# Optimization experiments

Measured on AMD Instinct MI355X. Metric: run time of the kernel, lower is better.

The kernel has to match this reference:

```python
import jax, jax.numpy as jnp
import numpy as np

S = 3072        # total packed tokens
E = 1280        # d_model
H = 20          # encoder_attention_heads
D = E // H      # head_dim = 64
NSEG = 16       # number of packed audio chunks


def setup_inputs() -> dict:
    key = jax.random.key(0)
    ks = jax.random.split(key, 9)
    w = lambda k, shape: (jax.random.normal(k, shape, jnp.float32) * 0.02)
    hidden_states = jax.random.normal(ks[0], (S, E), jnp.float32)
    cu_seqlens = (jnp.arange(NSEG + 1, dtype=jnp.int32) * (S // NSEG))
    return {
        "hidden_states": hidden_states,
        "Wq": w(ks[1], (E, E)), "bq": w(ks[2], (E,)),
        "Wk": w(ks[3], (E, E)),                      # k_proj has no bias
        "Wv": w(ks[4], (E, E)), "bv": w(ks[5], (E,)),
        "Wo": w(ks[6], (E, E)), "bo": w(ks[7], (E,)),
        "cu_seqlens": cu_seqlens,
    }


def reference(hidden_states, Wq, bq, Wk, Wv, bv, Wo, bo, cu_seqlens):
    Sq, Em = hidden_states.shape
    Dh = Em // H
    # projections (torch Linear: x @ W.T + b)
    q = (hidden_states @ Wq.T + bq).reshape(Sq, H, Dh).transpose(1, 0, 2)  # [H,S,D]
    k = (hidden_states @ Wk.T).reshape(Sq, H, Dh).transpose(1, 0, 2)       # [H,S,D]
    v = (hidden_states @ Wv.T + bv).reshape(Sq, H, Dh).transpose(1, 0, 2)  # [H,S,D]
    # block-diagonal additive mask from cu_seqlens (vectorized equivalent of
    # the original Python loop): tokens attend only within their own segment.
    pos = jnp.arange(Sq)
    seg = jnp.searchsorted(cu_seqlens[1:], pos, side="right")              # segment id per token
    same = seg[:, None] == seg[None, :]                                    # [S,S]
    bias = jnp.where(same, 0.0, jnp.finfo(q.dtype).min)
    attn = jnp.einsum("hqd,hkd->hqk", q, k) / np.sqrt(Dh).astype(q.dtype)  # [H,S,S]
    attn = jax.nn.softmax(attn + bias, axis=-1)
    out = jnp.einsum("hqk,hkd->hqd", attn, v)                              # [H,S,D]
    out = out.transpose(1, 0, 2).reshape(Sq, Em)
    return out @ Wo.T + bo
```

## Files before the change

kernel.cpp:

```cpp
#include <hip/hip_runtime.h>
#include <hip/hip_bf16.h>
#include <stdint.h>

#define S_TOK 3072
#define E_DIM 1280
#define H_NUM 20
#define D_HEAD 64
#define NSEG 16

typedef __attribute__((ext_vector_type(8))) short short8;
typedef __attribute__((ext_vector_type(4))) float f32x4;

__device__ __forceinline__ unsigned short f2bf(float f){
  union { float f; unsigned int i; } u; u.f = f;
  unsigned int r = u.i + 0x7FFFu + ((u.i >> 16) & 1u);
  return (unsigned short)(r >> 16);
}

__device__ __forceinline__ void gload_lds16(const void* g, void* l){
  __builtin_amdgcn_global_load_lds((__attribute__((address_space(1))) void*)(g),
                                   (__attribute__((address_space(3))) void*)(l), 16, 0, 0);
}

__global__ void cvt_all(const float* __restrict__ hs,
                        const float* __restrict__ w0, const float* __restrict__ w1,
                        const float* __restrict__ w2,
                        unsigned short* __restrict__ hsb,
                        unsigned short* __restrict__ dqkv,
                        int nHS4, int nW4){
  int i = blockIdx.x * blockDim.x + threadIdx.x;
  const float* src;
  unsigned short* dst;
  size_t sj, dj;
  if (i < nHS4){
    src = hs; dst = hsb; sj = i; dj = i;
  } else {
    int t = i - nHS4;
    int w = t / nW4;
    if (w >= 3) return;
    int j = t - w * nW4;
    src = (w == 0) ? w0 : (w == 1) ? w1 : w2;
    sj = j;
    dst = dqkv; dj = (size_t)w * nW4 + j;
  }
  float4 v = reinterpret_cast<const float4*>(src)[sj];
  ushort4 o;
  o.x = f2bf(v.x); o.y = f2bf(v.y); o.z = f2bf(v.z); o.w = f2bf(v.w);
  reinterpret_cast<ushort4*>(dst)[dj] = o;
}

template<int MODE, int BLOCK>
__global__ __launch_bounds__(BLOCK, 2) void gemm_k64(
    const unsigned short* __restrict__ A,
    const unsigned short* __restrict__ Bp,
    const float* __restrict__ bias0,
    const float* __restrict__ bias1,
    unsigned short* __restrict__ Oq,
    unsigned short* __restrict__ Ok,
    unsigned short* __restrict__ Ov,
    float* __restrict__ Of,
    int M, int N, int K)
{
  constexpr int BM = (MODE == 0) ? 256 : 128;
  constexpr int BN = BM;
  constexpr int WN = (MODE == 0) ? 4 : 2;
  constexpr int WM = (BLOCK / 64) / WN;
  constexpr int MR = BM / WM / 16;
  constexpr int NR = BN / WN / 16;
  constexpr int SLOT = (BM + BN) * 64;

  __shared__ __align__(16) unsigned short SH[2 * SLOT];

  const int nbn = N >> (MODE == 0 ? 8 : 7);
  const int sgn = nbn / 5;
  const int st = blockIdx.x / 20, ii = blockIdx.x % 20;
  const int bm = (st / sgn) * 4 + ii / 5;
  const int bn = (st % sgn) * 5 + ii % 5;
  const int row0 = bm * BM;
  const int col0 = bn * BN;

  const int tid  = threadIdx.x;
  const int lane = tid & 63;
  const int w    = tid >> 6;
  const int wm   = (MODE == 0) ? (w >> 2) : (w >> 1);
  const int wn   = (MODE == 0) ? (w & 3) : (w & 1);

  const f32x4 fz = {0.f, 0.f, 0.f, 0.f};
  f32x4 acc[MR][NR];
#pragma unroll
  for (int m = 0; m < MR; ++m)
#pragma unroll
    for (int n = 0; n < NR; ++n) acc[m][n] = fz;

  auto stage = [&](int buf, int t){
    unsigned short* base = SH + buf * SLOT;
    const int k0 = t << 6;
#pragma unroll
    for (int i = 0; i < 8; ++i){
      int s = i * BLOCK + tid;
      int r = s >> 3, p = s & 7;
      int ks = p ^ (r & 7);
      const unsigned short* g = (r < BM)
          ? A  + (size_t)(row0 + r) * K + k0 + ks * 8
          : Bp + (size_t)(col0 + (r - BM)) * K + k0 + ks * 8;
      gload_lds16(g, base + s * 8);
    }
  };

  const int nk = K >> 6;
  stage(0, 0);
  int buf = 0;
  for (int t = 0; t < nk; ++t){
    asm volatile("s_waitcnt vmcnt(0)" ::: "memory");
    __builtin_amdgcn_s_barrier();
    if (t + 1 < nk) stage(buf ^ 1, t + 1);

    const unsigned short* As = SH + buf * SLOT;
    const unsigned short* Bs = As + BM * 64;
    short8 af[MR][2], bf[NR][2];
#pragma unroll
    for (int n = 0; n < NR; ++n){
      int rb = wn * (BN / WN) + n * 16 + (lane & 15);
#pragma unroll
      for (int kk = 0; kk < 2; ++kk){
        int slot = kk * 4 + (lane >> 4);
        bf[n][kk] = *reinterpret_cast<const short8*>(&Bs[rb * 64 + ((slot ^ (rb & 7))) * 8]);
      }
    }
#pragma unroll
    for (int m = 0; m < MR; ++m){
      int ra = wm * (BM / WM) + m * 16 + (lane & 15);
#pragma unroll
      for (int kk = 0; kk < 2; ++kk){
        int slot = kk * 4 + (lane >> 4);
        af[m][kk] = *reinterpret_cast<const short8*>(&As[ra * 64 + ((slot ^ (ra & 7))) * 8]);
      }
    }
    __builtin_amdgcn_s_setprio(1);
#pragma unroll
    for (int kk = 0; kk < 2; ++kk)
#pragma unroll
      for (int m = 0; m < MR; ++m)
#pragma unroll
        for (int n = 0; n < NR; ++n)
          acc[m][n] = __builtin_amdgcn_mfma_f32_16x16x32_bf16(af[m][kk], bf[n][kk], acc[m][n], 0, 0, 0);
    __builtin_amdgcn_s_setprio(0);
    buf ^= 1;
  }
  __syncthreads();

  if (MODE == 0){
    unsigned short* Cs = SH;
    const int CSTR = 264;
    const int mat = col0 / E_DIM;
    const int cc0 = col0 - mat * E_DIM;
    unsigned short* dst = (mat == 0) ? Oq : ((mat == 1) ? Ok : Ov);
    float bb[NR];
#pragma unroll
    for (int n = 0; n < NR; ++n){
      int cc = cc0 + wn * 64 + n * 16 + (lane & 15);
      bb[n] = (mat == 0) ? bias0[cc] : (mat == 2 ? bias1[cc] : 0.0f);
    }
#pragma unroll
    for (int ph = 0; ph < 2; ++ph){
      if (wm == ph){
#pragma unroll
        for (int m = 0; m < MR; ++m)
#pragma unroll
          for (int n = 0; n < NR; ++n)
#pragma unroll
            for (int j = 0; j < 4; ++j){
              int rr = m * 16 + (lane >> 4) * 4 + j;
              int c  = wn * 64 + n * 16 + (lane & 15);
              Cs[rr * CSTR + c] = f2bf(acc[m][n][j] + bb[n]);
            }
      }
      __syncthreads();
#pragma unroll
      for (int i = 0; i < 8; ++i){
        int tk  = i * 512 + tid;
        int p   = tk >> 10;
        int idx = tk & 1023;
        int rr  = idx >> 3, sq = idx & 7;
        short8 vv = *reinterpret_cast<const short8*>(&Cs[rr * CSTR + p * 64 + sq * 8]);
        int gr = row0 + ph * 128 + rr;
        int hh = (cc0 >> 6) + p;
        *reinterpret_cast<short8*>(&dst[((size_t)hh * S_TOK + gr) * D_HEAD + sq * 8]) = vv;
      }
      __syncthreads();
    }
  } else {
#pragma unroll
    for (int m = 0; m < MR; ++m)
#pragma unroll
      for (int n = 0; n < NR; ++n){
        int c = col0 + wn * 64 + n * 16 + (lane & 15);
        float b = bias0[c];
#pragma unroll
        for (int j = 0; j < 4; ++j){
          int r = row0 + wm * 64 + m * 16 + (lane >> 4) * 4 + j;
          Of[(size_t)r * E_DIM + c] = acc[m][n][j] + b;
        }
      }
  }
}

#define VSTR 200
#define PSTR 72
#define ATTN_BLKS (H_NUM * NSEG * 3)
__global__ __launch_bounds__(256, 3) void attn_kernel(
    const unsigned short* __restrict__ Q,
    const unsigned short* __restrict__ Kb,
    const unsigned short* __restrict__ V,
    const int* __restrict__ cu,
    unsigned short* __restrict__ O,
    const float* __restrict__ Wo,
    unsigned short* __restrict__ wob,
    int nW4)
{
  __shared__ __align__(16) unsigned short Vt[64*VSTR];
  __shared__ __align__(16) unsigned short Pw[4][16][PSTR];

  const int bid  = blockIdx.x;
  if (bid >= ATTN_BLKS){
    int i = (bid - ATTN_BLKS) * 256 + threadIdx.x;
    if (i < nW4){
      float4 v = reinterpret_cast<const float4*>(Wo)[i];
      ushort4 o;
      o.x = f2bf(v.x); o.y = f2bf(v.y); o.z = f2bf(v.z); o.w = f2bf(v.w);
      reinterpret_cast<ushort4*>(wob)[i] = o;
    }
    return;
  }
  const int unit = bid / 3;
  const int third= bid - unit*3;
  const int h    = unit >> 4;
  const int seg  = unit & 15;
  const int s0   = cu[seg];
  const int L    = cu[seg + 1] - s0;
  if (L <= 0) return;

  const int tid  = threadIdx.x;
  const int lane = tid & 63;
  const int w    = tid >> 6;
  const int row0g = third*64 + w*16;

  const unsigned short* qh = Q  + (size_t)h * S_TOK * D_HEAD;
  const unsigned short* kh = Kb + (size_t)h * S_TOK * D_HEAD;
  const unsigned short* vh = V  + (size_t)h * S_TOK * D_HEAD;

#pragma unroll
  for (int i = 0; i < 6; ++i){
    int task = i*256 + tid;
    int sr   = task % 192;
    int grp  = task / 192;
    int svr  = s0 + (sr < L ? sr : L - 1);
    short8 vv = *reinterpret_cast<const short8*>(vh + (size_t)svr*64 + grp*8);
#pragma unroll
    for (int j = 0; j < 8; ++j) Vt[(grp*8 + j)*VSTR + sr] = (unsigned short)vv[j];
  }

  short8 qf[2];
#pragma unroll
  for (int kk = 0; kk < 2; ++kk){
    int r  = row0g + (lane & 15);
    int sr = s0 + (r < L ? r : L - 1);
    qf[kk] = *reinterpret_cast<const short8*>(qh + (size_t)sr*64 + kk*32 + (lane >> 4)*8);
  }

  __syncthreads();

  const f32x4 fz = {0.f, 0.f, 0.f, 0.f};
  const float SCL = 0.125f * 1.44269504088896f;

  f32x4 sacc[12];
#pragma unroll
  for (int nt = 0; nt < 12; ++nt) sacc[nt] = fz;

#pragma unroll
  for (int nt = 0; nt < 12; ++nt){
    int rb = nt*16 + (lane & 15);
    int sr = s0 + (rb < L ? rb : L - 1);
    const unsigned short* kr = kh + (size_t)sr*64 + (lane >> 4)*8;
    short8 kf0 = *reinterpret_cast<const short8*>(kr);
    short8 kf1 = *reinterpret_cast<const short8*>(kr + 32);
    sacc[nt] = __builtin_amdgcn_mfma_f32_16x16x32_bf16(qf[0], kf0, sacc[nt], 0, 0, 0);
    sacc[nt] = __builtin_amdgcn_mfma_f32_16x16x32_bf16(qf[1], kf1, sacc[nt], 0, 0, 0);
  }

  float rinv[4];
#pragma unroll
  for (int j = 0; j < 4; ++j){
    float mx = -1e30f;
#pragma unroll
    for (int nt = 0; nt < 12; ++nt){
      int c = nt*16 + (lane & 15);
      float vv = (c < L) ? sacc[nt][j] : -1e30f;
      sacc[nt][j] = vv;
      mx = fmaxf(mx, vv);
    }
    mx = fmaxf(mx, __shfl_xor(mx, 1, 64));
    mx = fmaxf(mx, __shfl_xor(mx, 2, 64));
    mx = fmaxf(mx, __shfl_xor(mx, 4, 64));
    mx = fmaxf(mx, __shfl_xor(mx, 8, 64));
    float sum = 0.f;
#pragma unroll
    for (int nt = 0; nt < 12; ++nt){
      float pp = exp2f((sacc[nt][j] - mx) * SCL);
      sacc[nt][j] = pp;
      sum += pp;
    }
    sum += __shfl_xor(sum, 1, 64);
    sum += __shfl_xor(sum, 2, 64);
    sum += __shfl_xor(sum, 4, 64);
    sum += __shfl_xor(sum, 8, 64);
    rinv[j] = 1.0f / sum;
  }

  f32x4 oacc[4];
#pragma unroll
  for (int nt = 0; nt < 4; ++nt) oacc[nt] = fz;

#pragma unroll
  for (int kk = 0; kk < 6; ++kk){
#pragma unroll
    for (int ntl = 0; ntl < 2; ++ntl){
      int nt = kk*2 + ntl;
#pragma unroll
      for (int j = 0; j < 4; ++j)
        Pw[w][(lane >> 4)*4 + j][ntl*16 + (lane & 15)] = f2bf(sacc[nt][j]);
    }
    short8 pf = *reinterpret_cast<const short8*>(&Pw[w][lane & 15][(lane >> 4)*8]);
#pragma unroll
    for (int nt4 = 0; nt4 < 4; ++nt4){
      int dcol = nt4*16 + (lane & 15);
      short8 vf = *reinterpret_cast<const short8*>(&Vt[dcol*VSTR + kk*32 + (lane >> 4)*8]);
      oacc[nt4] = __builtin_amdgcn_mfma_f32_16x16x32_bf16(pf, vf, oacc[nt4], 0, 0, 0);
    }
  }

#pragma unroll
  for (int nt4 = 0; nt4 < 4; ++nt4)
#pragma unroll
    for (int j = 0; j < 4; ++j)
      Pw[w][(lane >> 4)*4 + j][nt4*16 + (lane & 15)] = f2bf(oacc[nt4][j] * rinv[j]);

  {
    int r = lane >> 2;
    int gr = row0g + r;
    if (gr < L){
#pragma unroll
      for (int part = 0; part < 2; ++part){
        int c0 = (lane & 3)*16 + part*8;
        short8 vv = *reinterpret_cast<const short8*>(&Pw[w][r][c0]);
        *reinterpret_cast<short8*>(&O[(size_t)(s0 + gr) * E_DIM + h*64 + c0]) = vv;
      }
    }
  }
}

extern "C" void kernel_launch(void* const* d_in, const int* in_sizes, int n_in,
                              void* d_out, int out_size, void* d_ws, size_t ws_size,
                              hipStream_t stream)
{
  const float* hs = (const float*)d_in[0];
  const float* Wq = (const float*)d_in[1];
  const float* bq = (const float*)d_in[2];
  const float* Wk = (const float*)d_in[3];
  const float* Wv = (const float*)d_in[4];
  const float* bv = (const float*)d_in[5];
  const float* Wo = (const float*)d_in[6];
  const float* bo = (const float*)d_in[7];
  const int*   cu = (const int*)d_in[8];
  float* out = (float*)d_out;

  unsigned short* p = (unsigned short*)d_ws;
  unsigned short* hsb  = p; p += (size_t)S_TOK * E_DIM;
  unsigned short* wqkv = p; p += (size_t)3 * E_DIM * E_DIM;
  unsigned short* wob  = p; p += (size_t)E_DIM * E_DIM;
  unsigned short* qb   = p; p += (size_t)S_TOK * E_DIM;
  unsigned short* kb   = p; p += (size_t)S_TOK * E_DIM;
  unsigned short* vb   = p; p += (size_t)S_TOK * E_DIM;
  unsigned short* aob  = p; p += (size_t)S_TOK * E_DIM;

  const int nHS4 = S_TOK * E_DIM / 4;
  const int nW4  = E_DIM * E_DIM / 4;
  const int nCvt = nHS4 + 3 * nW4;
  cvt_all<<<(nCvt + 255) / 256, 256, 0, stream>>>(hs, Wq, Wk, Wv, hsb, wqkv, nHS4, nW4);

  gemm_k64<0, 512><<<(S_TOK/256) * (3*E_DIM/256), 512, 0, stream>>>(
      hsb, wqkv, bq, bv, qb, kb, vb, nullptr, S_TOK, 3*E_DIM, E_DIM);

  const int cvtWoBlks = (nW4 + 255) / 256;
  attn_kernel<<<ATTN_BLKS + cvtWoBlks, 256, 0, stream>>>(
      qb, kb, vb, cu, aob, Wo, wob, nW4);

  gemm_k64<1, 256><<<(S_TOK/128) * (E_DIM/128), 256, 0, stream>>>(
      aob, wob, bo, nullptr, nullptr, nullptr, nullptr, out, S_TOK, E_DIM, E_DIM);
}
```

Measured before the change: 97.75 us.

## Split GEMM tiles into half-quadrants with interleaved staged loads and XCD-aware remap

Rewrites both projection GEMMs so each K-step loads A and B as halves and computes four accumulator quadrants in turn. The next step's half-tiles are issued between quadrants, with partial vmcnt waits and extra barriers, so global-to-LDS loads overlap with MFMA work instead of waiting for a full tile each step. Workgroup IDs are also remapped so consecutive tiles land on the same XCD, which should help L2 reuse. The cost is more barriers and more complex wait counting, and getting the quadrant-to-output mapping wrong would produce incorrect results.

New measurement: 93.76 us. 1.04x faster.

```diff
diff --git a/kernel.cpp b/kernel.cpp
--- a/kernel.cpp
+++ b/kernel.cpp
@@ -49,8 +49,8 @@
   reinterpret_cast<ushort4*>(dst)[dj] = o;
 }
 
-template<int MODE, int BLOCK>
-__global__ __launch_bounds__(BLOCK, 2) void gemm_k64(
+template<int MODE>
+__global__ __launch_bounds__(MODE==0?512:256, 2) void gemm_ph(
     const unsigned short* __restrict__ A,
     const unsigned short* __restrict__ Bp,
     const float* __restrict__ bias0,
@@ -61,91 +61,129 @@
     float* __restrict__ Of,
     int M, int N, int K)
 {
-  constexpr int BM = (MODE == 0) ? 256 : 128;
-  constexpr int BN = BM;
-  constexpr int WN = (MODE == 0) ? 4 : 2;
-  constexpr int WM = (BLOCK / 64) / WN;
-  constexpr int MR = BM / WM / 16;
-  constexpr int NR = BN / WN / 16;
-  constexpr int SLOT = (BM + BN) * 64;
-
-  __shared__ __align__(16) unsigned short SH[2 * SLOT];
-
-  const int nbn = N >> (MODE == 0 ? 8 : 7);
+  constexpr int BM    = MODE==0 ? 256 : 128;
+  constexpr int BLOCK = MODE==0 ? 512 : 256;
+  constexpr int HR    = BM/2;
+  constexpr int HS    = HR*64;
+  constexpr int MR2   = MODE==0 ? 4 : 2;
+
+  __shared__ __align__(16) unsigned short SH[8*HS];
+
+  const int nwg = gridDim.x;
+  const int xcd = blockIdx.x & 7, ix = blockIdx.x >> 3;
+  const int qq = nwg >> 3, rr8 = nwg & 7;
+  const int wg = (xcd < rr8 ? xcd*(qq+1) : rr8*(qq+1) + (xcd-rr8)*qq) + ix;
+  const int nbn = N / BM;
   const int sgn = nbn / 5;
-  const int st = blockIdx.x / 20, ii = blockIdx.x % 20;
+  const int st = wg / 20, ii = wg % 20;
   const int bm = (st / sgn) * 4 + ii / 5;
   const int bn = (st % sgn) * 5 + ii % 5;
-  const int row0 = bm * BM;
-  const int col0 = bn * BN;
+  const int row0 = bm * BM, col0 = bn * BM;
 
   const int tid  = threadIdx.x;
   const int lane = tid & 63;
   const int w    = tid >> 6;
-  const int wm   = (MODE == 0) ? (w >> 2) : (w >> 1);
-  const int wn   = (MODE == 0) ? (w & 3) : (w & 1);
+  const int wm   = MODE==0 ? (w >> 2) : (w >> 1);
+  const int wn   = MODE==0 ? (w & 3) : (w & 1);
 
   const f32x4 fz = {0.f, 0.f, 0.f, 0.f};
-  f32x4 acc[MR][NR];
-#pragma unroll
-  for (int m = 0; m < MR; ++m)
-#pragma unroll
-    for (int n = 0; n < NR; ++n) acc[m][n] = fz;
-
-  auto stage = [&](int buf, int t){
-    unsigned short* base = SH + buf * SLOT;
-    const int k0 = t << 6;
-#pragma unroll
-    for (int i = 0; i < 8; ++i){
-      int s = i * BLOCK + tid;
-      int r = s >> 3, p = s & 7;
-      int ks = p ^ (r & 7);
-      const unsigned short* g = (r < BM)
-          ? A  + (size_t)(row0 + r) * K + k0 + ks * 8
-          : Bp + (size_t)(col0 + (r - BM)) * K + k0 + ks * 8;
-      gload_lds16(g, base + s * 8);
-    }
+  f32x4 acc[4][MR2][2];
+#pragma unroll
+  for (int qd = 0; qd < 4; ++qd)
+#pragma unroll
+    for (int m = 0; m < MR2; ++m)
+#pragma unroll
+      for (int n = 0; n < 2; ++n) acc[qd][m][n] = fz;
+
+  const int s1 = tid, s2 = BLOCK + tid;
+  const int r1 = s1 >> 3, ks1 = (s1 & 7) ^ (r1 & 7);
+  const int r2 = s2 >> 3, ks2 = (s2 & 7) ^ (r2 & 7);
+
+  auto stA = [&](int h, int t){
+    unsigned short* d = SH + ((t & 1) * 4 + h) * HS;
+    const unsigned short* g = A + (size_t)(row0 + h*HR) * K + (t << 6);
+    gload_lds16(g + (size_t)r1*K + ks1*8, d + s1*8);
+    gload_lds16(g + (size_t)r2*K + ks2*8, d + s2*8);
   };
+  auto stB = [&](int h, int t){
+    unsigned short* d = SH + ((t & 1) * 4 + 2 + h) * HS;
+    const unsigned short* g = Bp + (size_t)(col0 + h*HR) * K + (t << 6);
+    gload_lds16(g + (size_t)r1*K + ks1*8, d + s1*8);
+    gload_lds16(g + (size_t)r2*K + ks2*8, d + s2*8);
+  };
+
+  short8 af[MR2][2], bf0[2][2], bf1[2][2];
+  auto RA = [&](int mh, int db){
+    const unsigned short* Ah = SH + (db*4 + mh)*HS;
+#pragma unroll
+    for (int m = 0; m < MR2; ++m){
+      int ra = wm*(HR/2) + m*16 + (lane & 15);
+#pragma unroll
+      for (int kk = 0; kk < 2; ++kk){
+        int sl = kk*4 + (lane >> 4);
+        af[m][kk] = *reinterpret_cast<const short8*>(&Ah[ra*64 + ((sl ^ (ra & 7)))*8]);
+      }
+    }
+  };
+  auto RB = [&](int nh, int db, short8 (*bf)[2]){
+    const unsigned short* Bh = SH + (db*4 + 2 + nh)*HS;
+#pragma unroll
+    for (int n = 0; n < 2; ++n){
+      int rb = wn*32 + n*16 + (lane & 15);
+#pragma unroll
+      for (int kk = 0; kk < 2; ++kk){
+        int sl = kk*4 + (lane >> 4);
+        bf[n][kk] = *reinterpret_cast<const short8*>(&Bh[rb*64 + ((sl ^ (rb & 7)))*8]);
+      }
+    }
+  };
+
+#define MF_Q(QD, BF)                                                          \
+  do {                                                                        \
+    __builtin_amdgcn_s_setprio(1);                                            \
+    _Pragma("unroll")                                                         \
+    for (int kk = 0; kk < 2; ++kk)                                            \
+      _Pragma("unroll")                                                       \
+      for (int m = 0; m < MR2; ++m)                                           \
+        _Pragma("unroll")                                                     \
+        for (int n = 0; n < 2; ++n)                                           \
+          acc[QD][m][n] = __builtin_amdgcn_mfma_f32_16x16x32_bf16(            \
+              af[m][kk], BF[n][kk], acc[QD][m][n], 0, 0, 0);                  \
+    __builtin_amdgcn_s_setprio(0);                                            \
+  } while (0)
 
   const int nk = K >> 6;
-  stage(0, 0);
-  int buf = 0;
+  stA(0,0); stB(0,0); stB(1,0); stA(1,0);
+
   for (int t = 0; t < nk; ++t){
-    asm volatile("s_waitcnt vmcnt(0)" ::: "memory");
+    const int db = t & 1;
+    const bool nx = (t + 1 < nk);
+    asm volatile("s_waitcnt vmcnt(4)" ::: "memory");
     __builtin_amdgcn_s_barrier();
-    if (t + 1 < nk) stage(buf ^ 1, t + 1);
-
-    const unsigned short* As = SH + buf * SLOT;
-    const unsigned short* Bs = As + BM * 64;
-    short8 af[MR][2], bf[NR][2];
-#pragma unroll
-    for (int n = 0; n < NR; ++n){
-      int rb = wn * (BN / WN) + n * 16 + (lane & 15);
-#pragma unroll
-      for (int kk = 0; kk < 2; ++kk){
-        int slot = kk * 4 + (lane >> 4);
-        bf[n][kk] = *reinterpret_cast<const short8*>(&Bs[rb * 64 + ((slot ^ (rb & 7))) * 8]);
-      }
-    }
-#pragma unroll
-    for (int m = 0; m < MR; ++m){
-      int ra = wm * (BM / WM) + m * 16 + (lane & 15);
-#pragma unroll
-      for (int kk = 0; kk < 2; ++kk){
-        int slot = kk * 4 + (lane >> 4);
-        af[m][kk] = *reinterpret_cast<const short8*>(&As[ra * 64 + ((slot ^ (ra & 7))) * 8]);
-      }
-    }
-    __builtin_amdgcn_s_setprio(1);
-#pragma unroll
-    for (int kk = 0; kk < 2; ++kk)
-#pragma unroll
-      for (int m = 0; m < MR; ++m)
-#pragma unroll
-        for (int n = 0; n < NR; ++n)
-          acc[m][n] = __builtin_amdgcn_mfma_f32_16x16x32_bf16(af[m][kk], bf[n][kk], acc[m][n], 0, 0, 0);
-    __builtin_amdgcn_s_setprio(0);
-    buf ^= 1;
+    RA(0, db); RB(0, db, bf0);
+    if (nx) stA(0, t+1);
+    asm volatile("s_waitcnt lgkmcnt(0)" ::: "memory");
+    __builtin_amdgcn_sched_barrier(0);
+    MF_Q(0, bf0);
+    if (nx) asm volatile("s_waitcnt vmcnt(4)" ::: "memory");
+    else    asm volatile("s_waitcnt vmcnt(2)" ::: "memory");
+    __builtin_amdgcn_s_barrier();
+    RB(1, db, bf1);
+    if (nx) stB(0, t+1);
+    asm volatile("s_waitcnt lgkmcnt(0)" ::: "memory");
+    __builtin_amdgcn_sched_barrier(0);
+    MF_Q(1, bf1);
+    if (nx) asm volatile("s_waitcnt vmcnt(4)" ::: "memory");
+    else    asm volatile("s_waitcnt vmcnt(0)" ::: "memory");
+    __builtin_amdgcn_s_barrier();
+    RA(1, db);
+    if (nx) stB(1, t+1);
+    asm volatile("s_waitcnt lgkmcnt(0)" ::: "memory");
+    __builtin_amdgcn_sched_barrier(0);
+    MF_Q(2, bf1);
+    __builtin_amdgcn_s_barrier();
+    if (nx) stA(1, t+1);
+    MF_Q(3, bf0);
   }
   __syncthreads();
 
@@ -155,24 +193,29 @@
     const int mat = col0 / E_DIM;
     const int cc0 = col0 - mat * E_DIM;
     unsigned short* dst = (mat == 0) ? Oq : ((mat == 1) ? Ok : Ov);
-    float bb[NR];
-#pragma unroll
-    for (int n = 0; n < NR; ++n){
-      int cc = cc0 + wn * 64 + n * 16 + (lane & 15);
-      bb[n] = (mat == 0) ? bias0[cc] : (mat == 2 ? bias1[cc] : 0.0f);
-    }
+    float bb[2][2];
+#pragma unroll
+    for (int nh = 0; nh < 2; ++nh)
+#pragma unroll
+      for (int n = 0; n < 2; ++n){
+        int cc = cc0 + nh*128 + wn*32 + n*16 + (lane & 15);
+        bb[nh][n] = (mat == 0) ? bias0[cc] : (mat == 2 ? bias1[cc] : 0.0f);
+      }
 #pragma unroll
     for (int ph = 0; ph < 2; ++ph){
-      if (wm == ph){
-#pragma unroll
-        for (int m = 0; m < MR; ++m)
-#pragma unroll
-          for (int n = 0; n < NR; ++n)
+#pragma unroll
+      for (int q2i = 0; q2i < 2; ++q2i){
+        const int qd = ph*2 + q2i;
+        const int nh = (qd >> 1) ^ (qd & 1);
+#pragma unroll
+        for (int m = 0; m < MR2; ++m)
+#pragma unroll
+          for (int n = 0; n < 2; ++n)
 #pragma unroll
             for (int j = 0; j < 4; ++j){
-              int rr = m * 16 + (lane >> 4) * 4 + j;
-              int c  = wn * 64 + n * 16 + (lane & 15);
-              Cs[rr * CSTR + c] = f2bf(acc[m][n][j] + bb[n]);
+              int rr = wm*64 + m*16 + (lane >> 4)*4 + j;
+              int c  = nh*128 + wn*32 + n*16 + (lane & 15);
+              Cs[rr * CSTR + c] = f2bf(acc[qd][m][n][j] + bb[nh][n]);
             }
       }
       __syncthreads();
@@ -190,19 +233,30 @@
       __syncthreads();
     }
   } else {
-#pragma unroll
-    for (int m = 0; m < MR; ++m)
-#pragma unroll
-      for (int n = 0; n < NR; ++n){
-        int c = col0 + wn * 64 + n * 16 + (lane & 15);
-        float b = bias0[c];
-#pragma unroll
-        for (int j = 0; j < 4; ++j){
-          int r = row0 + wm * 64 + m * 16 + (lane >> 4) * 4 + j;
-          Of[(size_t)r * E_DIM + c] = acc[m][n][j] + b;
+    float bc[2][2];
+#pragma unroll
+    for (int nh = 0; nh < 2; ++nh)
+#pragma unroll
+      for (int n = 0; n < 2; ++n)
+        bc[nh][n] = bias0[col0 + nh*64 + wn*32 + n*16 + (lane & 15)];
+#pragma unroll
+    for (int qd = 0; qd < 4; ++qd){
+      const int mh = qd >> 1;
+      const int nh = (qd >> 1) ^ (qd & 1);
+#pragma unroll
+      for (int m = 0; m < MR2; ++m)
+#pragma unroll
+        for (int n = 0; n < 2; ++n){
+          int c = col0 + nh*64 + wn*32 + n*16 + (lane & 15);
+#pragma unroll
+          for (int j = 0; j < 4; ++j){
+            int r = row0 + mh*64 + wm*32 + m*16 + (lane >> 4)*4 + j;
+            Of[(size_t)r * E_DIM + c] = acc[qd][m][n][j] + bc[nh][n];
+          }
         }
-      }
-  }
+    }
+  }
+#undef MF_Q
 }
 
 #define VSTR 200
@@ -388,13 +442,13 @@
   const int nCvt = nHS4 + 3 * nW4;
   cvt_all<<<(nCvt + 255) / 256, 256, 0, stream>>>(hs, Wq, Wk, Wv, hsb, wqkv, nHS4, nW4);
 
-  gemm_k64<0, 512><<<(S_TOK/256) * (3*E_DIM/256), 512, 0, stream>>>(
+  gemm_ph<0><<<(S_TOK/256) * (3*E_DIM/256), 512, 0, stream>>>(
       hsb, wqkv, bq, bv, qb, kb, vb, nullptr, S_TOK, 3*E_DIM, E_DIM);
 
   const int cvtWoBlks = (nW4 + 255) / 256;
   attn_kernel<<<ATTN_BLKS + cvtWoBlks, 256, 0, stream>>>(
       qb, kb, vb, cu, aob, Wo, wob, nW4);
 
-  gemm_k64<1, 256><<<(S_TOK/128) * (E_DIM/128), 256, 0, stream>>>(
+  gemm_ph<1><<<(S_TOK/128) * (E_DIM/128), 256, 0, stream>>>(
       aob, wob, bo, nullptr, nullptr, nullptr, nullptr, out, S_TOK, E_DIM, E_DIM);
 }
```
